# Kernel tuning notes

Hardware: AMD Instinct MI355X
Metric: run time of the kernel (lower is better)

## Reference

```python
import jax, jax.numpy as jnp
import numpy as np

B, F, H, E, O = 512, 512, 512, 8, 512  # batch, feature, hidden, experts, out_frame


def setup_inputs() -> dict:
    key = jax.random.key(0)
    ks = jax.random.split(key, 14)
    u = lambda k, shape, s: jax.random.uniform(k, shape, jnp.float32) * s
    return {
        "x": jax.random.normal(ks[0], (B, F), jnp.float32),
        # gating MLP params (torch Linear: y = x @ W.T + b)
        "gw0": u(ks[1], (H, F), 0.04) - 0.02,
        "gb0": jnp.zeros((H,), jnp.float32),
        "gw1": u(ks[2], (H, H), 0.04) - 0.02,
        "gb1": jnp.zeros((H,), jnp.float32),
        "gw2": u(ks[3], (E, H), 0.04) - 0.02,
        "gb2": jnp.zeros((E,), jnp.float32),
        # expert weight/bias banks
        "alpha0": u(ks[4], (E, H, F), 0.01),
        "beta0": jnp.zeros((E, H, 1), jnp.float32),
        "alpha1": u(ks[5], (E, H, H), 0.01),
        "beta1": jnp.zeros((E, H, 1), jnp.float32),
        "alpha2": u(ks[6], (E, O, H), 0.01),
        "beta2": jnp.zeros((E, O, 1), jnp.float32),
    }


def reference(x, gw0, gb0, gw1, gb1, gw2, gb2,
              alpha0, beta0, alpha1, beta1, alpha2, beta2):
    # gating network
    h = jax.nn.elu(x @ gw0.T + gb0)
    h = jax.nn.elu(h @ gw1.T + gb1)
    g = jax.nn.softmax(h @ gw2.T + gb2, axis=1)  # [B, E]

    # per-sample blended weights (sum over experts of gate-scaled expert mats)
    blend_w = lambda a: jnp.einsum('be,ehf->bhf', g, a)
    blend_b = lambda b: jnp.einsum('be,eh->bh', g, b[..., 0])

    # per-sample 3-layer MLP (bmm with vector rhs == batched matvec)
    H1 = jax.nn.elu(jnp.einsum('bhf,bf->bh', blend_w(alpha0), x) + blend_b(beta0))
    H2 = jax.nn.elu(jnp.einsum('bhf,bf->bh', blend_w(alpha1), H1) + blend_b(beta1))
    H3 = jnp.einsum('bof,bf->bo', blend_w(alpha2), H2) + blend_b(beta2)
    return H3
```

## Files before the change

kernel.cpp:

```cpp
#include <hip/hip_runtime.h>
#include <hip/hip_bf16.h>
#include <math.h>

enum { Bq = 512, Fq = 512, Hq = 512, Eq = 8, Oq = 512 };

typedef __attribute__((ext_vector_type(8))) short short8;
typedef __attribute__((ext_vector_type(4))) float floatx4;

static __device__ __forceinline__ unsigned short f2bf(float f) {
  unsigned u = __float_as_uint(f);
  u += 0x7fffu + ((u >> 16) & 1u);
  return (unsigned short)(u >> 16);
}
static __device__ __forceinline__ float bf2f(unsigned short h) {
  return __uint_as_float(((unsigned)h) << 16);
}
static __device__ __forceinline__ float elu1(float v) {
  return v > 0.f ? v : (__expf(v) - 1.f);
}

typedef __attribute__((address_space(1))) const unsigned int gu32;
typedef __attribute__((address_space(3))) unsigned int lu32;
static __device__ __forceinline__ void gld16(const unsigned short* g,
                                             unsigned short* l) {
  __builtin_amdgcn_global_load_lds((gu32*)g, (lu32*)l, 16, 0, 0);
}

static __device__ __forceinline__ int swz(int q, int r) {
  return (q & ~7) | ((q ^ r) & 7);
}

static __device__ __forceinline__ void cvt_chunk(const float* __restrict__ src,
                                                 unsigned short* __restrict__ dst,
                                                 int chunk, int tid) {
  int j = chunk * 256 + tid;
  float4 v = ((const float4*)src)[j];
  ushort4 o;
  o.x = f2bf(v.x); o.y = f2bf(v.y); o.z = f2bf(v.z); o.w = f2bf(v.w);
  *(ushort4*)(dst + 4 * (size_t)j) = o;
}

__global__ __launch_bounds__(256) void cvt_small(
    const float* __restrict__ s0, const float* __restrict__ s1,
    const float* __restrict__ s2, unsigned short* __restrict__ d0,
    unsigned short* __restrict__ d1, unsigned short* __restrict__ d2) {
  int blk = blockIdx.x;
  int seg = blk >> 8, c = blk & 255;
  const float* s = (seg == 0) ? s0 : (seg == 1) ? s1 : s2;
  unsigned short* d = (seg == 0) ? d0 : (seg == 1) ? d1 : d2;
  cvt_chunk(s, d, c, threadIdx.x);
}

__global__ __launch_bounds__(256) void gating_cvt(
    const unsigned short* __restrict__ A, const unsigned short* __restrict__ W,
    const float* __restrict__ bias, unsigned short* __restrict__ C,
    const float* __restrict__ asrc, unsigned short* __restrict__ adst) {
  const int blk = blockIdx.x, tid = threadIdx.x;
  if (blk >= 256) {
    cvt_chunk(asrc, adst, blk - 256, tid);
    return;
  }
  __shared__ unsigned short As[32 * 512];
  __shared__ unsigned short Ws[32 * 512];
  const int wave = tid >> 6, lane = tid & 63;
  const int wm = wave >> 1, wn = wave & 1;
  const int lr = lane & 15, lk = lane >> 4;
  const int m0 = (blk >> 4) * 32, n0 = (blk & 15) * 32;
#pragma unroll
  for (int i = 0; i < 8; i++) {
    int c = tid + i * 256;
    int r = c >> 6, ql = c & 63;
    gld16(&A[(size_t)(m0 + r) * 512 + swz(ql, r) * 8], &As[(c & ~63) * 8]);
  }
#pragma unroll
  for (int i = 0; i < 8; i++) {
    int c = tid + i * 256;
    int r = c >> 6, ql = c & 63;
    gld16(&W[(size_t)(n0 + r) * 512 + swz(ql, r) * 8], &Ws[(c & ~63) * 8]);
  }
  __syncthreads();
  const int rA = wm * 16 + lr, rB = wn * 16 + lr;
  floatx4 ac[4];
#pragma unroll
  for (int j = 0; j < 4; j++) ac[j] = (floatx4){0.f, 0.f, 0.f, 0.f};
#pragma unroll
  for (int t = 0; t < 4; t++) {
#pragma unroll
    for (int j = 0; j < 4; j++) {
      int q = ((j * 128 + t * 32) >> 3) + lk;
      short8 av = *(const short8*)&As[rA * 512 + swz(q, rA) * 8];
      short8 bv = *(const short8*)&Ws[rB * 512 + swz(q, rB) * 8];
      ac[j] = __builtin_amdgcn_mfma_f32_16x16x32_bf16(av, bv, ac[j], 0, 0, 0);
    }
  }
  floatx4 acc = (ac[0] + ac[1]) + (ac[2] + ac[3]);
  int n = n0 + wn * 16 + lr;
  float bn = bias[n];
#pragma unroll
  for (int r = 0; r < 4; r++) {
    int m = m0 + wm * 16 + lk * 4 + r;
    C[(size_t)m * 512 + n] = f2bf(elu1(acc[r] + bn));
  }
}

__global__ __launch_bounds__(256) void gate_fused(
    const unsigned short* __restrict__ G1,
    const float* __restrict__ gw2,
    const float* __restrict__ gb2,
    float* __restrict__ g,
    const float* __restrict__ asrc, unsigned short* __restrict__ adst,
    float* __restrict__ outz) {
  const int blk = blockIdx.x, tid = threadIdx.x;
  if (blk >= 384) {
    cvt_chunk(asrc, adst, blk - 384, tid);
    return;
  }
  if (blk >= 128) {
    ((float4*)outz)[(blk - 128) * 256 + tid] = (float4){0.f, 0.f, 0.f, 0.f};
    return;
  }
  const int wave = tid >> 6, lane = tid & 63;
  const int b = blk * 4 + wave;
  float xv[8];
#pragma unroll
  for (int t = 0; t < 8; t++) xv[t] = bf2f(G1[(size_t)b * Hq + t * 64 + lane]);
  float le[Eq];
#pragma unroll
  for (int e = 0; e < Eq; e++) {
    float p = 0.f;
#pragma unroll
    for (int t = 0; t < 8; t++)
      p += xv[t] * gw2[(size_t)e * Hq + t * 64 + lane];
#pragma unroll
    for (int o = 32; o > 0; o >>= 1) p += __shfl_xor(p, o);
    le[e] = p + gb2[e];
  }
  float m = le[0];
#pragma unroll
  for (int e = 1; e < Eq; e++) m = fmaxf(m, le[e]);
  float s = 0.f;
#pragma unroll
  for (int e = 0; e < Eq; e++) {
    le[e] = __expf(le[e] - m);
    s += le[e];
  }
  float inv = 1.f / s;
  if (lane == 0) {
#pragma unroll
    for (int e = 0; e < Eq; e++) g[(size_t)b * Eq + e] = le[e] * inv;
  }
}

template <int FROMP, int ATOMIC>
__global__ __launch_bounds__(256) void expert_gemm(
    const unsigned short* __restrict__ A,
    const float* __restrict__ Pin,
    const unsigned short* __restrict__ Wb,
    const float* __restrict__ g,
    const float* __restrict__ beta,
    float* __restrict__ Pout) {
  __shared__ unsigned short As[32 * 256];
  __shared__ unsigned short Ws[2][32 * 256];
  const int tid = threadIdx.x;
  const int wave = tid >> 6, lane = tid & 63;
  const int wm = wave >> 1, wn = wave & 1;
  const int lr = lane & 15, lk = lane >> 4;
  const int m0 = blockIdx.y * 32, n0 = blockIdx.x * 32;
  const int kz = blockIdx.z, kbeg = kz * 256;

  if (FROMP) {
#pragma unroll
    for (int i = 0; i < 4; i++) {
      int c = tid + i * 256;
      int r = c >> 5, q = c & 31;
      const float* p0 = Pin + (size_t)(m0 + r) * 512 + kbeg + q * 8;
      const float* p1 = p0 + (size_t)Bq * Hq;
      float4 x0 = *(const float4*)p0, x1 = *(const float4*)(p0 + 4);
      float4 y0 = *(const float4*)p1, y1 = *(const float4*)(p1 + 4);
      short8 o;
      o[0] = (short)f2bf(elu1(x0.x + y0.x));
      o[1] = (short)f2bf(elu1(x0.y + y0.y));
      o[2] = (short)f2bf(elu1(x0.z + y0.z));
      o[3] = (short)f2bf(elu1(x0.w + y0.w));
      o[4] = (short)f2bf(elu1(x1.x + y1.x));
      o[5] = (short)f2bf(elu1(x1.y + y1.y));
      o[6] = (short)f2bf(elu1(x1.z + y1.z));
      o[7] = (short)f2bf(elu1(x1.w + y1.w));
      *(short8*)&As[(r * 32 + swz(q, r)) * 8] = o;
    }
  } else {
#pragma unroll
    for (int i = 0; i < 4; i++) {
      int c = tid + i * 256;
      int r = c >> 5, ql = c & 31;
      gld16(&A[(size_t)(m0 + r) * 512 + kbeg + swz(ql, r) * 8],
            &As[(c & ~63) * 8]);
    }
  }
  auto stageW = [&](int e, int b) {
    const unsigned short* Wp = Wb + ((size_t)e * 512 + n0) * 512 + kbeg;
#pragma unroll
    for (int i = 0; i < 4; i++) {
      int c = tid + i * 256;
      int r = c >> 5, ql = c & 31;
      gld16(&Wp[(size_t)r * 512 + swz(ql, r) * 8], &Ws[b][(c & ~63) * 8]);
    }
  };
  stageW(0, 0);
  float g8[4][8];
#pragma unroll
  for (int r = 0; r < 4; r++) {
    int m = m0 + wm * 16 + lk * 4 + r;
    float4 ga = *(const float4*)&g[(size_t)m * 8];
    float4 gb = *(const float4*)&g[(size_t)m * 8 + 4];
    g8[r][0] = ga.x; g8[r][1] = ga.y; g8[r][2] = ga.z; g8[r][3] = ga.w;
    g8[r][4] = gb.x; g8[r][5] = gb.y; g8[r][6] = gb.z; g8[r][7] = gb.w;
  }

  const int rA = wm * 16 + lr, rB = wn * 16 + lr;
  floatx4 fin = {0.f, 0.f, 0.f, 0.f};
#pragma unroll
  for (int e = 0; e < 8; e++) {
    __syncthreads();
    if (e < 7) stageW(e + 1, (e + 1) & 1);
    const unsigned short* wb = Ws[e & 1];
    floatx4 c0 = {0.f, 0.f, 0.f, 0.f}, c1 = {0.f, 0.f, 0.f, 0.f};
#pragma unroll
    for (int s = 0; s < 8; s++) {
      int q = s * 4 + lk;
      short8 av = *(const short8*)&As[rA * 256 + swz(q, rA) * 8];
      short8 bv = *(const short8*)&wb[rB * 256 + swz(q, rB) * 8];
      if (s & 1)
        c1 = __builtin_amdgcn_mfma_f32_16x16x32_bf16(av, bv, c1, 0, 0, 0);
      else
        c0 = __builtin_amdgcn_mfma_f32_16x16x32_bf16(av, bv, c0, 0, 0, 0);
    }
    floatx4 ae = c0 + c1;
#pragma unroll
    for (int r = 0; r < 4; r++) fin[r] += g8[r][e] * ae[r];
  }

  int n = n0 + wn * 16 + lr;
  if (kz == 0) {
    float bv[8];
#pragma unroll
    for (int e = 0; e < 8; e++) bv[e] = beta[e * 512 + n];
#pragma unroll
    for (int r = 0; r < 4; r++) {
      float bs = 0.f;
#pragma unroll
      for (int e = 0; e < 8; e++) bs += g8[r][e] * bv[e];
      fin[r] += bs;
    }
  }
  if (ATOMIC) {
#pragma unroll
    for (int r = 0; r < 4; r++) {
      int m = m0 + wm * 16 + lk * 4 + r;
      atomicAdd(&Pout[(size_t)m * 512 + n], fin[r]);
    }
  } else {
    float* Po = Pout + (size_t)kz * Bq * Hq;
#pragma unroll
    for (int r = 0; r < 4; r++) {
      int m = m0 + wm * 16 + lk * 4 + r;
      Po[(size_t)m * 512 + n] = fin[r];
    }
  }
}

extern "C" void kernel_launch(void* const* d_in, const int* in_sizes, int n_in,
                              void* d_out, int out_size, void* d_ws,
                              size_t ws_size, hipStream_t stream) {
  const float* x = (const float*)d_in[0];
  const float* gw0 = (const float*)d_in[1];
  const float* gb0 = (const float*)d_in[2];
  const float* gw1 = (const float*)d_in[3];
  const float* gb1 = (const float*)d_in[4];
  const float* gw2 = (const float*)d_in[5];
  const float* gb2 = (const float*)d_in[6];
  const float* alpha0 = (const float*)d_in[7];
  const float* beta0 = (const float*)d_in[8];
  const float* alpha1 = (const float*)d_in[9];
  const float* beta1 = (const float*)d_in[10];
  const float* alpha2 = (const float*)d_in[11];
  const float* beta2 = (const float*)d_in[12];
  float* out = (float*)d_out;

  char* ws = (char*)d_ws;
  auto alloc = [&](size_t bytes) {
    char* p = ws;
    ws += (bytes + 255) & ~(size_t)255;
    return p;
  };
  unsigned short* xb = (unsigned short*)alloc((size_t)Bq * Fq * 2);
  unsigned short* gw0b = (unsigned short*)alloc((size_t)Hq * Fq * 2);
  unsigned short* gw1b = (unsigned short*)alloc((size_t)Hq * Hq * 2);
  unsigned short* a0b = (unsigned short*)alloc((size_t)Eq * Hq * Fq * 2);
  unsigned short* a1b = (unsigned short*)alloc((size_t)Eq * Hq * Hq * 2);
  unsigned short* a2b = (unsigned short*)alloc((size_t)Eq * Oq * Hq * 2);
  unsigned short* G0b = (unsigned short*)alloc((size_t)Bq * Hq * 2);
  unsigned short* G1b = (unsigned short*)alloc((size_t)Bq * Hq * 2);
  float* gates = (float*)alloc((size_t)Bq * Eq * 4);
  float* P1 = (float*)alloc((size_t)2 * Bq * Hq * 4);
  float* P2 = (float*)alloc((size_t)2 * Bq * Hq * 4);

  cvt_small<<<768, 256, 0, stream>>>(x, gw0, gw1, xb, gw0b, gw1b);

  gating_cvt<<<2304, 256, 0, stream>>>(xb, gw0b, gb0, G0b, alpha0, a0b);
  gating_cvt<<<2304, 256, 0, stream>>>(G0b, gw1b, gb1, G1b, alpha1, a1b);

  gate_fused<<<2432, 256, 0, stream>>>(G1b, gw2, gb2, gates, alpha2, a2b, out);

  dim3 ge(16, 16, 2);
  expert_gemm<0, 0><<<ge, 256, 0, stream>>>(xb, nullptr, a0b, gates, beta0, P1);
  expert_gemm<1, 0><<<ge, 256, 0, stream>>>(nullptr, P1, a1b, gates, beta1, P2);
  expert_gemm<1, 1><<<ge, 256, 0, stream>>>(nullptr, P2, a2b, gates, beta2, out);
}
```

Before: 136.1 us.

## Fuse gate softmax into first expert GEMM and redistribute side work across launches

Removes the separate gating-softmax kernel. Each block of the first expert GEMM now recomputes the softmax gates for its 32 rows into shared memory, and one block column also writes them to global memory for the later layers. The alpha2 conversion, output zeroing and gw1 conversion are moved into the spare blocks of other launches, so there is one fewer kernel launch and the expert GEMM grids are better filled. The cost is redundant gate computation in every block and extra latency before the MFMA loop starts.

After: 163.4 us. +20.1%, slower.

```diff
diff --git a/kernel.cpp b/kernel.cpp
--- a/kernel.cpp
+++ b/kernel.cpp
@@ -40,22 +40,26 @@
   *(ushort4*)(dst + 4 * (size_t)j) = o;
 }
 
-__global__ __launch_bounds__(256) void cvt_small(
+__global__ __launch_bounds__(256) void cvt_small2(
     const float* __restrict__ s0, const float* __restrict__ s1,
-    const float* __restrict__ s2, unsigned short* __restrict__ d0,
-    unsigned short* __restrict__ d1, unsigned short* __restrict__ d2) {
+    unsigned short* __restrict__ d0, unsigned short* __restrict__ d1) {
   int blk = blockIdx.x;
-  int seg = blk >> 8, c = blk & 255;
-  const float* s = (seg == 0) ? s0 : (seg == 1) ? s1 : s2;
-  unsigned short* d = (seg == 0) ? d0 : (seg == 1) ? d1 : d2;
-  cvt_chunk(s, d, c, threadIdx.x);
+  if (blk < 256)
+    cvt_chunk(s0, d0, blk, threadIdx.x);
+  else
+    cvt_chunk(s1, d1, blk - 256, threadIdx.x);
 }
 
 __global__ __launch_bounds__(256) void gating_cvt(
     const unsigned short* __restrict__ A, const unsigned short* __restrict__ W,
     const float* __restrict__ bias, unsigned short* __restrict__ C,
-    const float* __restrict__ asrc, unsigned short* __restrict__ adst) {
+    const float* __restrict__ asrc, unsigned short* __restrict__ adst,
+    const float* __restrict__ ssrc, unsigned short* __restrict__ sdst) {
   const int blk = blockIdx.x, tid = threadIdx.x;
+  if (blk >= 2304) {
+    cvt_chunk(ssrc, sdst, blk - 2304, tid);
+    return;
+  }
   if (blk >= 256) {
     cvt_chunk(asrc, adst, blk - 256, tid);
     return;
@@ -103,70 +107,35 @@
   }
 }
 
-__global__ __launch_bounds__(256) void gate_fused(
-    const unsigned short* __restrict__ G1,
-    const float* __restrict__ gw2,
-    const float* __restrict__ gb2,
-    float* __restrict__ g,
-    const float* __restrict__ asrc, unsigned short* __restrict__ adst,
-    float* __restrict__ outz) {
-  const int blk = blockIdx.x, tid = threadIdx.x;
-  if (blk >= 384) {
-    cvt_chunk(asrc, adst, blk - 384, tid);
-    return;
-  }
-  if (blk >= 128) {
-    ((float4*)outz)[(blk - 128) * 256 + tid] = (float4){0.f, 0.f, 0.f, 0.f};
-    return;
-  }
-  const int wave = tid >> 6, lane = tid & 63;
-  const int b = blk * 4 + wave;
-  float xv[8];
-#pragma unroll
-  for (int t = 0; t < 8; t++) xv[t] = bf2f(G1[(size_t)b * Hq + t * 64 + lane]);
-  float le[Eq];
-#pragma unroll
-  for (int e = 0; e < Eq; e++) {
-    float p = 0.f;
-#pragma unroll
-    for (int t = 0; t < 8; t++)
-      p += xv[t] * gw2[(size_t)e * Hq + t * 64 + lane];
-#pragma unroll
-    for (int o = 32; o > 0; o >>= 1) p += __shfl_xor(p, o);
-    le[e] = p + gb2[e];
-  }
-  float m = le[0];
-#pragma unroll
-  for (int e = 1; e < Eq; e++) m = fmaxf(m, le[e]);
-  float s = 0.f;
-#pragma unroll
-  for (int e = 0; e < Eq; e++) {
-    le[e] = __expf(le[e] - m);
-    s += le[e];
-  }
-  float inv = 1.f / s;
-  if (lane == 0) {
-#pragma unroll
-    for (int e = 0; e < Eq; e++) g[(size_t)b * Eq + e] = le[e] * inv;
-  }
-}
-
-template <int FROMP, int ATOMIC>
+template <int FROMP, int ATOMIC, int GATES, int EXTRA>
 __global__ __launch_bounds__(256) void expert_gemm(
     const unsigned short* __restrict__ A,
     const float* __restrict__ Pin,
     const unsigned short* __restrict__ Wb,
-    const float* __restrict__ g,
+    float* __restrict__ gates,
     const float* __restrict__ beta,
-    float* __restrict__ Pout) {
+    float* __restrict__ Pout,
+    const unsigned short* __restrict__ G1,
+    const float* __restrict__ gw2, const float* __restrict__ gb2,
+    const float* __restrict__ xsrc, unsigned short* __restrict__ xdst,
+    float* __restrict__ zdst) {
+  const int id = blockIdx.x, tid = threadIdx.x;
+  if (EXTRA == 1 && id >= 512) {
+    cvt_chunk(xsrc, xdst, id - 512, tid);
+    return;
+  }
+  if (EXTRA == 2 && id >= 512) {
+    ((float4*)zdst)[(id - 512) * 256 + tid] = (float4){0.f, 0.f, 0.f, 0.f};
+    return;
+  }
   __shared__ unsigned short As[32 * 256];
   __shared__ unsigned short Ws[2][32 * 256];
-  const int tid = threadIdx.x;
+  __shared__ float gl[32 * 8];
   const int wave = tid >> 6, lane = tid & 63;
   const int wm = wave >> 1, wn = wave & 1;
   const int lr = lane & 15, lk = lane >> 4;
-  const int m0 = blockIdx.y * 32, n0 = blockIdx.x * 32;
-  const int kz = blockIdx.z, kbeg = kz * 256;
+  const int xib = id & 15, yib = (id >> 4) & 15, kz = id >> 8;
+  const int n0 = xib * 32, m0 = yib * 32, kbeg = kz * 256;
 
   if (FROMP) {
 #pragma unroll
@@ -207,14 +176,56 @@
     }
   };
   stageW(0, 0);
+
   float g8[4][8];
-#pragma unroll
-  for (int r = 0; r < 4; r++) {
-    int m = m0 + wm * 16 + lk * 4 + r;
-    float4 ga = *(const float4*)&g[(size_t)m * 8];
-    float4 gb = *(const float4*)&g[(size_t)m * 8 + 4];
-    g8[r][0] = ga.x; g8[r][1] = ga.y; g8[r][2] = ga.z; g8[r][3] = ga.w;
-    g8[r][4] = gb.x; g8[r][5] = gb.y; g8[r][6] = gb.z; g8[r][7] = gb.w;
+  if (GATES) {
+#pragma unroll
+    for (int rr = 0; rr < 8; rr++) {
+      int row = wave * 8 + rr;
+      int m = m0 + row;
+      float xv[8];
+#pragma unroll
+      for (int t = 0; t < 8; t++)
+        xv[t] = bf2f(G1[(size_t)m * 512 + t * 64 + lane]);
+      float le[8];
+#pragma unroll
+      for (int e = 0; e < 8; e++) {
+        float p = 0.f;
+#pragma unroll
+        for (int t = 0; t < 8; t++)
+          p += xv[t] * gw2[(size_t)e * 512 + t * 64 + lane];
+#pragma unroll
+        for (int o = 32; o > 0; o >>= 1) p += __shfl_xor(p, o);
+        le[e] = p + gb2[e];
+      }
+      float mm = le[0];
+#pragma unroll
+      for (int e = 1; e < 8; e++) mm = fmaxf(mm, le[e]);
+      float s = 0.f;
+#pragma unroll
+      for (int e = 0; e < 8; e++) {
+        le[e] = __expf(le[e] - mm);
+        s += le[e];
+      }
+      float inv = 1.f / s;
+      if (lane == 0) {
+#pragma unroll
+        for (int e = 0; e < 8; e++) {
+          float gv = le[e] * inv;
+          gl[row * 8 + e] = gv;
+          if (xib == 0 && kz == 0) gates[(size_t)m * 8 + e] = gv;
+        }
+      }
+    }
+  } else {
+#pragma unroll
+    for (int r = 0; r < 4; r++) {
+      int m = m0 + wm * 16 + lk * 4 + r;
+      float4 ga = *(const float4*)&gates[(size_t)m * 8];
+      float4 gb = *(const float4*)&gates[(size_t)m * 8 + 4];
+      g8[r][0] = ga.x; g8[r][1] = ga.y; g8[r][2] = ga.z; g8[r][3] = ga.w;
+      g8[r][4] = gb.x; g8[r][5] = gb.y; g8[r][6] = gb.z; g8[r][7] = gb.w;
+    }
   }
 
   const int rA = wm * 16 + lr, rB = wn * 16 + lr;
@@ -237,7 +248,10 @@
     }
     floatx4 ae = c0 + c1;
 #pragma unroll
-    for (int r = 0; r < 4; r++) fin[r] += g8[r][e] * ae[r];
+    for (int r = 0; r < 4; r++) {
+      float ge = GATES ? gl[(wm * 16 + lk * 4 + r) * 8 + e] : g8[r][e];
+      fin[r] += ge * ae[r];
+    }
   }
 
   int n = n0 + wn * 16 + lr;
@@ -249,7 +263,10 @@
     for (int r = 0; r < 4; r++) {
       float bs = 0.f;
 #pragma unroll
-      for (int e = 0; e < 8; e++) bs += g8[r][e] * bv[e];
+      for (int e = 0; e < 8; e++) {
+        float ge = GATES ? gl[(wm * 16 + lk * 4 + r) * 8 + e] : g8[r][e];
+        bs += ge * bv[e];
+      }
       fin[r] += bs;
     }
   }
@@ -305,15 +322,19 @@
   float* P1 = (float*)alloc((size_t)2 * Bq * Hq * 4);
   float* P2 = (float*)alloc((size_t)2 * Bq * Hq * 4);
 
-  cvt_small<<<768, 256, 0, stream>>>(x, gw0, gw1, xb, gw0b, gw1b);
-
-  gating_cvt<<<2304, 256, 0, stream>>>(xb, gw0b, gb0, G0b, alpha0, a0b);
-  gating_cvt<<<2304, 256, 0, stream>>>(G0b, gw1b, gb1, G1b, alpha1, a1b);
-
-  gate_fused<<<2432, 256, 0, stream>>>(G1b, gw2, gb2, gates, alpha2, a2b, out);
-
-  dim3 ge(16, 16, 2);
-  expert_gemm<0, 0><<<ge, 256, 0, stream>>>(xb, nullptr, a0b, gates, beta0, P1);
-  expert_gemm<1, 0><<<ge, 256, 0, stream>>>(nullptr, P1, a1b, gates, beta1, P2);
-  expert_gemm<1, 1><<<ge, 256, 0, stream>>>(nullptr, P2, a2b, gates, beta2, out);
-}
+  cvt_small2<<<512, 256, 0, stream>>>(x, gw0, xb, gw0b);
+
+  gating_cvt<<<2560, 256, 0, stream>>>(xb, gw0b, gb0, G0b, alpha0, a0b,
+                                       gw1, gw1b);
+  gating_cvt<<<2304, 256, 0, stream>>>(G0b, gw1b, gb1, G1b, alpha1, a1b,
+                                       nullptr, nullptr);
+
+  expert_gemm<0, 0, 1, 1><<<2560, 256, 0, stream>>>(
+      xb, nullptr, a0b, gates, beta0, P1, G1b, gw2, gb2, alpha2, a2b, nullptr);
+  expert_gemm<1, 0, 0, 2><<<768, 256, 0, stream>>>(
+      nullptr, P1, a1b, gates, beta1, P2, nullptr, nullptr, nullptr, nullptr,
+      nullptr, out);
+  expert_gemm<1, 1, 0, 0><<<512, 256, 0, stream>>>(
+      nullptr, P2, a2b, gates, beta2, out, nullptr, nullptr, nullptr, nullptr,
+      nullptr, nullptr);
+}
```
